# Kernel tuning notes

Measured on AMD Instinct MI355X. Metric: run time of the kernel, lower is better.

## Reference

```python
import jax, jax.numpy as jnp
import numpy as np

DIM = 512
HEADS = 8
DIM_HEAD = 64
INNER = HEADS * DIM_HEAD  # 512


def setup_inputs() -> dict:
    key = jax.random.key(0)
    k1, k2, k3, k4 = jax.random.split(key, 4)
    x = jax.random.normal(k1, (2, 2048, DIM), dtype=jnp.float32)
    # nn.Linear weights are [out_features, in_features]
    w_qkv = jax.random.normal(k2, (INNER * 3, DIM), dtype=jnp.float32) * (1.0 / np.sqrt(DIM))
    w_out = jax.random.normal(k3, (DIM, INNER), dtype=jnp.float32) * (1.0 / np.sqrt(INNER))
    b_out = jax.random.normal(k4, (DIM,), dtype=jnp.float32) * 0.01
    return {"x": x, "w_qkv": w_qkv, "w_out": w_out, "b_out": b_out}


def reference(x, w_qkv, w_out, b_out):
    b, n, _ = x.shape
    qkv = x @ w_qkv.T  # (b, n, 3*inner)
    q, k, v = jnp.split(qkv, 3, axis=-1)
    # (b, n, inner) -> (b, h, n, dh)
    def to_heads(t):
        return t.reshape(b, n, HEADS, DIM_HEAD).transpose(0, 2, 1, 3)
    q, k, v = map(to_heads, (q, k, v))
    # Faithful to the torch code: softmax over head dim for q, over seq for k
    q = jax.nn.softmax(q, axis=-1)
    k = jax.nn.softmax(k, axis=-2)
    # torch einsum labels seq as i/j, head dim as d (contracted) -> [n, n] context
    context = jnp.einsum('bhid,bhjd->bhij', k, v)     # (b, h, n, n)
    out = jnp.einsum('bhij,bhie->bhje', context, q)   # (b, h, n, dh)
    out = out.transpose(0, 2, 1, 3).reshape(b, n, INNER)
    return out @ w_out.T + b_out
```

## Files before the change

kernel.cpp:

```cpp
#include <hip/hip_runtime.h>
#include <hip/hip_bf16.h>
#include <math.h>

#define BB   2
#define NN   2048
#define DIMM 512
#define HH   8
#define NC3  1536
#define BN   4096

typedef __attribute__((ext_vector_type(8))) short short8;
typedef __attribute__((ext_vector_type(4))) float f32x4;
typedef unsigned short u16t;

__device__ inline short bfc(float f) {
    __hip_bfloat16 h = __float2bfloat16(f);
    return *reinterpret_cast<short*>(&h);
}
__device__ inline float bf2f(u16t u) {
    return __uint_as_float(((unsigned)u) << 16);
}

#define SWZ(P) ((P) ^ ((((P) >> 7) & 3) << 4))

__device__ inline void gll16(const u16t* gp, void* lp) {
    __builtin_amdgcn_global_load_lds(
        (const __attribute__((address_space(1))) void*)gp,
        (__attribute__((address_space(3))) void*)lp,
        16, 0, 0);
}

__global__ __launch_bounds__(256) void cvt_bf16(
    const float* __restrict__ x, const float* __restrict__ wq,
    u16t* __restrict__ xb, u16t* __restrict__ wqb)
{
    int t = blockIdx.x * 256 + threadIdx.x;
    const float4* src; ushort4* dst; int i;
    if (t < 524288) { src = (const float4*)x;  dst = (ushort4*)xb;  i = t; }
    else            { src = (const float4*)wq; dst = (ushort4*)wqb; i = t - 524288; }
    float4 v = src[i];
    ushort4 u;
    u.x = (u16t)bfc(v.x); u.y = (u16t)bfc(v.y);
    u.z = (u16t)bfc(v.z); u.w = (u16t)bfc(v.w);
    dst[i] = u;
}

__global__ __launch_bounds__(256) void qkvgemm(
    const u16t* __restrict__ A, const u16t* __restrict__ Bw,
    u16t* __restrict__ QKV)
{
    __shared__ __align__(16) char smem[32768];

    const int tid  = threadIdx.x;
    const int wave = tid >> 6, lane = tid & 63;
    const int wr = wave >> 1, wc = wave & 1;

    int bid = blockIdx.x;
    const int row0 = ((bid & 7) * 4 + ((bid >> 3) & 3)) * 128;
    const int c0   = (bid >> 5) * 128;

    size_t gA[2], gB[2];
#pragma unroll
    for (int j = 0; j < 2; ++j) {
        int c = wave * 2 + j;
        int X = (c * 64 + lane) * 16;
        int gi = SWZ(X) >> 4;
        int row = gi >> 2, col = (gi & 3) * 8;
        gA[j] = (size_t)(row0 + row) * DIMM + col;
        gB[j] = (size_t)(c0   + row) * DIMM + col;
    }

    int rdA[4], rdB[4];
#pragma unroll
    for (int i = 0; i < 4; ++i) {
        int Pa = (wr * 64 + i * 16 + (lane & 15)) * 64 + (lane >> 4) * 16;
        rdA[i] = SWZ(Pa);
        int Pb = (wc * 64 + i * 16 + (lane & 15)) * 64 + (lane >> 4) * 16;
        rdB[i] = 8192 + SWZ(Pb);
    }

#define QSTAGE(BUF, KT) {                                                     \
    char* sb = smem + (BUF) * 16384;                                          \
    _Pragma("unroll")                                                         \
    for (int j = 0; j < 2; ++j) {                                             \
        gll16(A  + gA[j] + (KT), sb + (wave * 2 + j) * 1024);                 \
        gll16(Bw + gB[j] + (KT), sb + 8192 + (wave * 2 + j) * 1024);          \
    } }

    f32x4 acc[4][4];
#pragma unroll
    for (int i = 0; i < 4; ++i)
#pragma unroll
        for (int j = 0; j < 4; ++j) acc[i][j] = (f32x4){0.f, 0.f, 0.f, 0.f};

    QSTAGE(0, 0);
    for (int t = 0; t < 16; ++t) {
        __syncthreads();
        if (t < 15) QSTAGE((t + 1) & 1, (t + 1) * 32);
        const char* rb = smem + (t & 1) * 16384;
        short8 af[4], bfr[4];
#pragma unroll
        for (int i = 0; i < 4; ++i) {
            af[i]  = *(const short8*)(rb + rdA[i]);
            bfr[i] = *(const short8*)(rb + rdB[i]);
        }
#pragma unroll
        for (int i = 0; i < 4; ++i)
#pragma unroll
            for (int j = 0; j < 4; ++j)
                acc[i][j] = __builtin_amdgcn_mfma_f32_16x16x32_bf16(
                    af[i], bfr[j], acc[i][j], 0, 0, 0);
    }
#undef QSTAGE

#pragma unroll
    for (int j = 0; j < 4; ++j) {
        int col = c0 + wc * 64 + j * 16 + (lane & 15);
#pragma unroll
        for (int i = 0; i < 4; ++i) {
#pragma unroll
            for (int r = 0; r < 4; ++r) {
                int row = row0 + wr * 64 + i * 16 + (lane >> 4) * 4 + r;
                QKV[(size_t)row * NC3 + col] = (u16t)bfc(acc[i][j][r]);
            }
        }
    }
}

#define TST 136

__global__ __launch_bounds__(512) void mpart(
    const u16t* __restrict__ QKV, float* __restrict__ Mp, float* __restrict__ ksump)
{
    __shared__ __align__(16) char sh[34816];
    u16t* ksT = (u16t*)sh;
    u16t* qsT = (u16t*)(sh + 17408);

    const int bh = blockIdx.x, ch = blockIdx.y;
    const int b = bh >> 3, h = bh & 7;
    const int tid = threadIdx.x;
    const u16t* base = QKV + ((size_t)b * NN + ch * 128) * NC3 + h * 64;

    const int k7 = tid & 7;
    const int d0 = k7 * 8;
    const int rr = tid >> 3;

#pragma unroll
    for (int pass = 0; pass < 2; ++pass) {
        int r = pass * 64 + rr;
        const u16t* rowp = base + (size_t)r * NC3 + d0;
        short8 qv = *(const short8*)(rowp);
        short8 kv = *(const short8*)(rowp + 512);
        float e[8]; float s = 0.f;
#pragma unroll
        for (int u = 0; u < 8; ++u) { e[u] = __expf(bf2f((u16t)qv[u])); s += e[u]; }
        s += __shfl_xor(s, 1); s += __shfl_xor(s, 2); s += __shfl_xor(s, 4);
        float inv = 1.0f / s;
        int gx = ((r >> 3) ^ k7) * 8 + (r & 7);
#pragma unroll
        for (int u = 0; u < 8; ++u)
            qsT[(d0 + u) * TST + gx] = (u16t)bfc(e[u] * inv);
#pragma unroll
        for (int u = 0; u < 8; ++u)
            ksT[(d0 + u) * TST + gx] = (u16t)bfc(__expf(bf2f((u16t)kv[u])));
    }
    __syncthreads();

    if (tid < 64) {
        float kss = 0.f;
#pragma unroll
        for (int gg = 0; gg < 16; ++gg) {
            short8 v = *(const short8*)(ksT + tid * TST + gg * 8);
#pragma unroll
            for (int u = 0; u < 8; ++u) kss += bf2f((u16t)v[u]);
        }
        ksump[(bh * 16 + ch) * 64 + tid] = kss;
    }

    const int wave = tid >> 6, lane = tid & 63;
    const int g = wave >> 1, kh = wave & 1;
    const int dl = lane & 15, kq = lane >> 4;
    const int d = g * 16 + dl;

    f32x4 acc[4];
#pragma unroll
    for (int j = 0; j < 4; ++j) acc[j] = (f32x4){0.f, 0.f, 0.f, 0.f};

#pragma unroll
    for (int ks2 = 0; ks2 < 2; ++ks2) {
        int kb = kh * 64 + ks2 * 32 + kq * 8;
        short8 af = *(const short8*)(ksT + d * TST + ((((kb >> 3) ^ (d >> 3))) << 3));
#pragma unroll
        for (int j = 0; j < 4; ++j) {
            int e = j * 16 + dl;
            short8 bfrj = *(const short8*)(qsT + e * TST + ((((kb >> 3) ^ (e >> 3))) << 3));
            acc[j] = __builtin_amdgcn_mfma_f32_16x16x32_bf16(af, bfrj, acc[j], 0, 0, 0);
        }
    }

    float* mp = Mp + ((size_t)((bh * 16 + ch) * 2 + kh)) * 4096;
#pragma unroll
    for (int j = 0; j < 4; ++j)
#pragma unroll
        for (int r = 0; r < 4; ++r)
            mp[(g * 16 + kq * 4 + r) * 64 + j * 16 + dl] = acc[j][r];
}

__global__ __launch_bounds__(256) void mreduce(
    const float* __restrict__ Mp, float* __restrict__ M)
{
    int bh = blockIdx.x;
    int idx = blockIdx.y * 256 + threadIdx.x;
    const float* p = Mp + (size_t)bh * 32 * 4096 + idx;
    float s = 0.f;
#pragma unroll
    for (int c = 0; c < 32; ++c) s += p[c * 4096];
    M[(size_t)bh * 4096 + idx] = s;
}

__global__ __launch_bounds__(256) void w2t(
    const float* __restrict__ M, const float* __restrict__ ksump,
    const float* __restrict__ w_out, u16t* __restrict__ W2T)
{
    __shared__ float kst[64];
    __shared__ float Ms[64][68];
    __shared__ float Wt[64][68];

    int bh = blockIdx.x, ot = blockIdx.y;
    int b = bh >> 3, h = bh & 7;
    int tid = threadIdx.x;
    int d = tid & 63, og = tid >> 6;

    if (tid < 64) {
        float s = 0.f;
#pragma unroll
        for (int c = 0; c < 16; ++c) s += ksump[(bh * 16 + c) * 64 + tid];
        kst[tid] = s;
    }
    for (int idx = tid; idx < 4096; idx += 256)
        Ms[idx >> 6][idx & 63] = M[(size_t)bh * 4096 + idx];
    {
        int o = tid >> 2, e0 = (tid & 3) * 16;
#pragma unroll
        for (int q = 0; q < 4; ++q)
            *(float4*)&Wt[o][e0 + q * 4] =
                *(const float4*)&w_out[(size_t)(ot * 64 + o) * DIMM + h * 64 + e0 + q * 4];
    }
    __syncthreads();

    float Mreg[64];
#pragma unroll
    for (int e4 = 0; e4 < 16; ++e4) {
        float4 v = *(const float4*)&Ms[d][e4 * 4];
        Mreg[e4 * 4 + 0] = v.x; Mreg[e4 * 4 + 1] = v.y;
        Mreg[e4 * 4 + 2] = v.z; Mreg[e4 * 4 + 3] = v.w;
    }
    float inv = 1.0f / kst[d];

#pragma unroll
    for (int oo = 0; oo < 16; ++oo) {
        int o = og * 16 + oo;
        float a = 0.f;
#pragma unroll
        for (int e4 = 0; e4 < 16; ++e4) {
            float4 wv = *(const float4*)&Wt[o][e4 * 4];
            a += wv.x * Mreg[e4 * 4 + 0] + wv.y * Mreg[e4 * 4 + 1]
               + wv.z * Mreg[e4 * 4 + 2] + wv.w * Mreg[e4 * 4 + 3];
        }
        W2T[((size_t)b * DIMM + ot * 64 + o) * DIMM + h * 64 + d] = (u16t)bfc(a * inv);
    }
}

__global__ __launch_bounds__(256) void outgemm(
    const u16t* __restrict__ Aq, const u16t* __restrict__ W2T,
    const float* __restrict__ bias, float* __restrict__ Out)
{
    __shared__ __align__(16) char smem[24576];

    const int tid  = threadIdx.x;
    const int wave = tid >> 6, lane = tid & 63;
    const int wr = wave >> 1, wc = wave & 1;

    int bid = blockIdx.x;
    const int row0 = ((bid & 7) * 4 + ((bid >> 3) & 3)) * 128;
    const int c0   = (bid >> 5) * 64;
    const u16t* Bp = W2T + (size_t)(row0 >> 11) * (DIMM * DIMM);

    size_t gA[2], gB;
#pragma unroll
    for (int j = 0; j < 2; ++j) {
        int c = wave * 2 + j;
        int gi = SWZ((c * 64 + lane) * 16) >> 4;
        int row = gi >> 2, col = (gi & 3) * 8;
        gA[j] = (size_t)(row0 + row) * NC3 + col;
    }
    {
        int gi = SWZ((wave * 64 + lane) * 16) >> 4;
        int row = gi >> 2, col = (gi & 3) * 8;
        gB = (size_t)(c0 + row) * DIMM + col;
    }

    int rdA[4], rdB[2];
#pragma unroll
    for (int i = 0; i < 4; ++i) {
        int Pa = (wr * 64 + i * 16 + (lane & 15)) * 64 + (lane >> 4) * 16;
        rdA[i] = SWZ(Pa);
    }
#pragma unroll
    for (int j = 0; j < 2; ++j) {
        int Pb = (wc * 32 + j * 16 + (lane & 15)) * 64 + (lane >> 4) * 16;
        rdB[j] = 8192 + SWZ(Pb);
    }

#define OSTAGE(BUF, KT) {                                                     \
    char* sb = smem + (BUF) * 12288;                                          \
    _Pragma("unroll")                                                         \
    for (int j = 0; j < 2; ++j)                                               \
        gll16(Aq + gA[j] + (KT), sb + (wave * 2 + j) * 1024);                 \
    gll16(Bp + gB + (KT), sb + 8192 + wave * 1024);                           \
    }

    f32x4 acc[4][2];
#pragma unroll
    for (int i = 0; i < 4; ++i)
#pragma unroll
        for (int j = 0; j < 2; ++j) acc[i][j] = (f32x4){0.f, 0.f, 0.f, 0.f};

    OSTAGE(0, 0);
    for (int t = 0; t < 16; ++t) {
        __syncthreads();
        if (t < 15) OSTAGE((t + 1) & 1, (t + 1) * 32);
        const char* rb = smem + (t & 1) * 12288;
        short8 af[4], bfr[2];
#pragma unroll
        for (int i = 0; i < 4; ++i) af[i]  = *(const short8*)(rb + rdA[i]);
#pragma unroll
        for (int j = 0; j < 2; ++j) bfr[j] = *(const short8*)(rb + rdB[j]);
#pragma unroll
        for (int i = 0; i < 4; ++i)
#pragma unroll
            for (int j = 0; j < 2; ++j)
                acc[i][j] = __builtin_amdgcn_mfma_f32_16x16x32_bf16(
                    af[i], bfr[j], acc[i][j], 0, 0, 0);
    }
#undef OSTAGE

#pragma unroll
    for (int j = 0; j < 2; ++j) {
        int col = c0 + wc * 32 + j * 16 + (lane & 15);
        float bb = bias[col];
#pragma unroll
        for (int i = 0; i < 4; ++i) {
#pragma unroll
            for (int r = 0; r < 4; ++r) {
                int row = row0 + wr * 64 + i * 16 + (lane >> 4) * 4 + r;
                Out[(size_t)row * DIMM + col] = acc[i][j][r] + bb;
            }
        }
    }
}

extern "C" void kernel_launch(void* const* d_in, const int* in_sizes, int n_in,
                              void* d_out, int out_size, void* d_ws, size_t ws_size,
                              hipStream_t stream)
{
    const float* x     = (const float*)d_in[0];
    const float* w_qkv = (const float*)d_in[1];
    const float* w_out = (const float*)d_in[2];
    const float* b_out = (const float*)d_in[3];
    float* out = (float*)d_out;

    char* w = (char*)d_ws;
    u16t*  xb   = (u16t*) (w);
    u16t*  wqb  = (u16t*) (w + 4194304);
    u16t*  QKV  = (u16t*) (w + 5767168);
    float* Mp   = (float*)(w + 18350080);
    float* ksum = (float*)(w + 26738688);
    float* Mm   = (float*)(w + 26804224);
    u16t*  W2T  = (u16t*) (w + 27066368);

    cvt_bf16<<<dim3(2816), 256, 0, stream>>>(x, w_qkv, xb, wqb);

    qkvgemm<<<dim3(384), 256, 0, stream>>>(xb, wqb, QKV);

    mpart<<<dim3(16, 16), 512, 0, stream>>>(QKV, Mp, ksum);

    mreduce<<<dim3(16, 16), 256, 0, stream>>>(Mp, Mm);

    w2t<<<dim3(16, 8), 256, 0, stream>>>(Mm, ksum, w_out, W2T);

    outgemm<<<dim3(256), 256, 0, stream>>>(QKV + 1024, W2T, b_out, out);
}
```

Baseline: 48.86 us.

## Fuse M reduction and W2T projection into one cooperative kernel with grid sync

Merges the mreduce and w2t kernels into a single cooperative launch of 256 blocks. A grid-wide sync separates the partial-sum reduction from the projection against w_out. The projection is also re-split so each block computes 32 output rows instead of 64, which doubles the block count for that phase. This removes one kernel launch and its gap, in exchange for the cost of a grid barrier and the constraints of a cooperative launch.

```diff
diff --git a/kernel.cpp b/kernel.cpp
--- a/kernel.cpp
+++ b/kernel.cpp
@@ -1,6 +1,9 @@
 #include <hip/hip_runtime.h>
 #include <hip/hip_bf16.h>
+#include <hip/hip_cooperative_groups.h>
 #include <math.h>
+
+namespace cg = cooperative_groups;
 
 #define BB   2
 #define NN   2048
@@ -206,30 +209,35 @@
             mp[(g * 16 + kq * 4 + r) * 64 + j * 16 + dl] = acc[j][r];
 }
 
-__global__ __launch_bounds__(256) void mreduce(
-    const float* __restrict__ Mp, float* __restrict__ M)
-{
-    int bh = blockIdx.x;
-    int idx = blockIdx.y * 256 + threadIdx.x;
-    const float* p = Mp + (size_t)bh * 32 * 4096 + idx;
-    float s = 0.f;
-#pragma unroll
-    for (int c = 0; c < 32; ++c) s += p[c * 4096];
-    M[(size_t)bh * 4096 + idx] = s;
-}
-
-__global__ __launch_bounds__(256) void w2t(
-    const float* __restrict__ M, const float* __restrict__ ksump,
-    const float* __restrict__ w_out, u16t* __restrict__ W2T)
-{
-    __shared__ float kst[64];
-    __shared__ float Ms[64][68];
-    __shared__ float Wt[64][68];
-
-    int bh = blockIdx.x, ot = blockIdx.y;
-    int b = bh >> 3, h = bh & 7;
-    int tid = threadIdx.x;
-    int d = tid & 63, og = tid >> 6;
+__global__ __launch_bounds__(256) void mw(
+    const float* __restrict__ Mp, float* __restrict__ Mm,
+    const float* __restrict__ ksump, const float* __restrict__ w_out,
+    u16t* __restrict__ W2T)
+{
+    __shared__ __align__(16) char sh[26368];
+    float* kst      = (float*)sh;
+    float (*Ms)[68] = (float(*)[68])(sh + 256);
+    float (*Wt)[68] = (float(*)[68])(sh + 17664);
+
+    const int bid = blockIdx.x;
+    const int tid = threadIdx.x;
+    const int bh = bid >> 4;
+    const int b = bh >> 3, h = bh & 7;
+
+    {
+        int idx = (bid & 15) * 256 + tid;
+        const float* p = Mp + (size_t)bh * 32 * 4096 + idx;
+        float s = 0.f;
+#pragma unroll
+        for (int c = 0; c < 32; ++c) s += p[c * 4096];
+        Mm[(size_t)bh * 4096 + idx] = s;
+    }
+
+    cg::this_grid().sync();
+
+    const int seg = bid & 15;
+    const int ob = seg * 32;
+    const int d = tid & 63, og = tid >> 6;
 
     if (tid < 64) {
         float s = 0.f;
@@ -237,14 +245,19 @@
         for (int c = 0; c < 16; ++c) s += ksump[(bh * 16 + c) * 64 + tid];
         kst[tid] = s;
     }
-    for (int idx = tid; idx < 4096; idx += 256)
-        Ms[idx >> 6][idx & 63] = M[(size_t)bh * 4096 + idx];
-    {
-        int o = tid >> 2, e0 = (tid & 3) * 16;
-#pragma unroll
-        for (int q = 0; q < 4; ++q)
-            *(float4*)&Wt[o][e0 + q * 4] =
-                *(const float4*)&w_out[(size_t)(ot * 64 + o) * DIMM + h * 64 + e0 + q * 4];
+#pragma unroll
+    for (int it = 0; it < 4; ++it) {
+        int idx4 = it * 256 + tid;
+        int dd = idx4 >> 4, e4 = idx4 & 15;
+        *(float4*)&Ms[dd][e4 * 4] =
+            *(const float4*)(Mm + (size_t)bh * 4096 + idx4 * 4);
+    }
+#pragma unroll
+    for (int it = 0; it < 2; ++it) {
+        int idx4 = it * 256 + tid;
+        int o = idx4 >> 4, e4 = idx4 & 15;
+        *(float4*)&Wt[o][e4 * 4] =
+            *(const float4*)&w_out[(size_t)(ob + o) * DIMM + h * 64 + e4 * 4];
     }
     __syncthreads();
 
@@ -258,8 +271,8 @@
     float inv = 1.0f / kst[d];
 
 #pragma unroll
-    for (int oo = 0; oo < 16; ++oo) {
-        int o = og * 16 + oo;
+    for (int oo = 0; oo < 8; ++oo) {
+        int o = og * 8 + oo;
         float a = 0.f;
 #pragma unroll
         for (int e4 = 0; e4 < 16; ++e4) {
@@ -267,7 +280,7 @@
             a += wv.x * Mreg[e4 * 4 + 0] + wv.y * Mreg[e4 * 4 + 1]
                + wv.z * Mreg[e4 * 4 + 2] + wv.w * Mreg[e4 * 4 + 3];
         }
-        W2T[((size_t)b * DIMM + ot * 64 + o) * DIMM + h * 64 + d] = (u16t)bfc(a * inv);
+        W2T[((size_t)b * DIMM + ob + o) * DIMM + h * 64 + d] = (u16t)bfc(a * inv);
     }
 }
 
@@ -385,9 +398,17 @@
 
     mpart<<<dim3(16, 16), 512, 0, stream>>>(QKV, Mp, ksum);
 
-    mreduce<<<dim3(16, 16), 256, 0, stream>>>(Mp, Mm);
-
-    w2t<<<dim3(16, 8), 256, 0, stream>>>(Mm, ksum, w_out, W2T);
+    {
+        const float* Mp_c = Mp;
+        float* Mm_c = Mm;
+        const float* ks_c = ksum;
+        const float* wo_c = w_out;
+        u16t* w2_c = W2T;
+        void* args[] = { (void*)&Mp_c, (void*)&Mm_c, (void*)&ks_c,
+                         (void*)&wo_c, (void*)&w2_c };
+        hipLaunchCooperativeKernel((const void*)mw, dim3(256), dim3(256),
+                                   args, 0, stream);
+    }
 
     outgemm<<<dim3(256), 256, 0, stream>>>(QKV + 1024, W2T, b_out, out);
 }
```

After: 79.67 us. 63.0% more time.

## Replace partial-M buffer and reduce kernel with atomic accumulation; split w2t finer

Applied to the files above, without the earlier changes.

mpart now atomically adds its partial 64x64 context products straight into a zeroed M buffer, which removes the large Mp scratch buffer and the separate mreduce launch. The zeroing is folded into the first 64 blocks of qkvgemm. w2t is also split into twice as many blocks, each handling 32 output columns, and its M tile is loaded with float4 reads. Float atomics make the summation order nondeterministic and add contention on each M tile.

```diff
diff --git a/kernel.cpp b/kernel.cpp
--- a/kernel.cpp
+++ b/kernel.cpp
@@ -47,7 +47,7 @@
 
 __global__ __launch_bounds__(256) void qkvgemm(
     const u16t* __restrict__ A, const u16t* __restrict__ Bw,
-    u16t* __restrict__ QKV)
+    u16t* __restrict__ QKV, float* __restrict__ Mm)
 {
     __shared__ __align__(16) char smem[32768];
 
@@ -56,6 +56,10 @@
     const int wr = wave >> 1, wc = wave & 1;
 
     int bid = blockIdx.x;
+    if (bid < 64) {
+        f32x4 z = (f32x4){0.f, 0.f, 0.f, 0.f};
+        ((f32x4*)Mm)[bid * 256 + tid] = z;
+    }
     const int row0 = ((bid & 7) * 4 + ((bid >> 3) & 3)) * 128;
     const int c0   = (bid >> 5) * 128;
 
@@ -130,7 +134,7 @@
 #define TST 136
 
 __global__ __launch_bounds__(512) void mpart(
-    const u16t* __restrict__ QKV, float* __restrict__ Mp, float* __restrict__ ksump)
+    const u16t* __restrict__ QKV, float* __restrict__ Mm, float* __restrict__ ksump)
 {
     __shared__ __align__(16) char sh[34816];
     u16t* ksT = (u16t*)sh;
@@ -198,38 +202,27 @@
         }
     }
 
-    float* mp = Mp + ((size_t)((bh * 16 + ch) * 2 + kh)) * 4096;
+    float* mm = Mm + (size_t)bh * 4096;
 #pragma unroll
     for (int j = 0; j < 4; ++j)
 #pragma unroll
         for (int r = 0; r < 4; ++r)
-            mp[(g * 16 + kq * 4 + r) * 64 + j * 16 + dl] = acc[j][r];
-}
-
-__global__ __launch_bounds__(256) void mreduce(
-    const float* __restrict__ Mp, float* __restrict__ M)
-{
-    int bh = blockIdx.x;
-    int idx = blockIdx.y * 256 + threadIdx.x;
-    const float* p = Mp + (size_t)bh * 32 * 4096 + idx;
-    float s = 0.f;
-#pragma unroll
-    for (int c = 0; c < 32; ++c) s += p[c * 4096];
-    M[(size_t)bh * 4096 + idx] = s;
+            atomicAdd(&mm[(g * 16 + kq * 4 + r) * 64 + j * 16 + dl], acc[j][r]);
 }
 
 __global__ __launch_bounds__(256) void w2t(
-    const float* __restrict__ M, const float* __restrict__ ksump,
+    const float* __restrict__ Mm, const float* __restrict__ ksump,
     const float* __restrict__ w_out, u16t* __restrict__ W2T)
 {
     __shared__ float kst[64];
     __shared__ float Ms[64][68];
-    __shared__ float Wt[64][68];
-
-    int bh = blockIdx.x, ot = blockIdx.y;
-    int b = bh >> 3, h = bh & 7;
-    int tid = threadIdx.x;
-    int d = tid & 63, og = tid >> 6;
+    __shared__ float Wt[32][68];
+
+    const int bh = blockIdx.x, ot = blockIdx.y;
+    const int b = bh >> 3, h = bh & 7;
+    const int tid = threadIdx.x;
+    const int d = tid & 63, og = tid >> 6;
+    const int ob = ot * 32;
 
     if (tid < 64) {
         float s = 0.f;
@@ -237,14 +230,19 @@
         for (int c = 0; c < 16; ++c) s += ksump[(bh * 16 + c) * 64 + tid];
         kst[tid] = s;
     }
-    for (int idx = tid; idx < 4096; idx += 256)
-        Ms[idx >> 6][idx & 63] = M[(size_t)bh * 4096 + idx];
+#pragma unroll
+    for (int it = 0; it < 4; ++it) {
+        int idx4 = it * 256 + tid;
+        int dd = idx4 >> 4, e4 = idx4 & 15;
+        *(float4*)&Ms[dd][e4 * 4] =
+            *(const float4*)(Mm + (size_t)bh * 4096 + idx4 * 4);
+    }
     {
-        int o = tid >> 2, e0 = (tid & 3) * 16;
-#pragma unroll
-        for (int q = 0; q < 4; ++q)
-            *(float4*)&Wt[o][e0 + q * 4] =
-                *(const float4*)&w_out[(size_t)(ot * 64 + o) * DIMM + h * 64 + e0 + q * 4];
+        int o = tid >> 3, e0 = (tid & 7) * 8;
+        *(float4*)&Wt[o][e0] =
+            *(const float4*)&w_out[(size_t)(ob + o) * DIMM + h * 64 + e0];
+        *(float4*)&Wt[o][e0 + 4] =
+            *(const float4*)&w_out[(size_t)(ob + o) * DIMM + h * 64 + e0 + 4];
     }
     __syncthreads();
 
@@ -258,8 +256,8 @@
     float inv = 1.0f / kst[d];
 
 #pragma unroll
-    for (int oo = 0; oo < 16; ++oo) {
-        int o = og * 16 + oo;
+    for (int oo = 0; oo < 8; ++oo) {
+        int o = og * 8 + oo;
         float a = 0.f;
 #pragma unroll
         for (int e4 = 0; e4 < 16; ++e4) {
@@ -267,7 +265,7 @@
             a += wv.x * Mreg[e4 * 4 + 0] + wv.y * Mreg[e4 * 4 + 1]
                + wv.z * Mreg[e4 * 4 + 2] + wv.w * Mreg[e4 * 4 + 3];
         }
-        W2T[((size_t)b * DIMM + ot * 64 + o) * DIMM + h * 64 + d] = (u16t)bfc(a * inv);
+        W2T[((size_t)b * DIMM + ob + o) * DIMM + h * 64 + d] = (u16t)bfc(a * inv);
     }
 }
 
@@ -374,20 +372,17 @@
     u16t*  xb   = (u16t*) (w);
     u16t*  wqb  = (u16t*) (w + 4194304);
     u16t*  QKV  = (u16t*) (w + 5767168);
-    float* Mp   = (float*)(w + 18350080);
-    float* ksum = (float*)(w + 26738688);
-    float* Mm   = (float*)(w + 26804224);
-    u16t*  W2T  = (u16t*) (w + 27066368);
+    float* Mm   = (float*)(w + 18350080);
+    float* ksum = (float*)(w + 18612224);
+    u16t*  W2T  = (u16t*) (w + 18677760);
 
     cvt_bf16<<<dim3(2816), 256, 0, stream>>>(x, w_qkv, xb, wqb);
 
-    qkvgemm<<<dim3(384), 256, 0, stream>>>(xb, wqb, QKV);
-
-    mpart<<<dim3(16, 16), 512, 0, stream>>>(QKV, Mp, ksum);
-
-    mreduce<<<dim3(16, 16), 256, 0, stream>>>(Mp, Mm);
-
-    w2t<<<dim3(16, 8), 256, 0, stream>>>(Mm, ksum, w_out, W2T);
+    qkvgemm<<<dim3(384), 256, 0, stream>>>(xb, wqb, QKV, Mm);
+
+    mpart<<<dim3(16, 16), 512, 0, stream>>>(QKV, Mm, ksum);
+
+    w2t<<<dim3(16, 16), 256, 0, stream>>>(Mm, ksum, w_out, W2T);
 
     outgemm<<<dim3(256), 256, 0, stream>>>(QKV + 1024, W2T, b_out, out);
 }
```

After: 48.07 us, median of 2. No clear change (-1.6%).
